# Kernel optimization log

Hardware: AMD Instinct MI355X
Metric: run time of the kernel (lower is better)

## Reference

```python
import jax, jax.numpy as jnp
import numpy as np

N_NODES = 100000   # m for both sparse matmuls (graph adjacency is N x N)
ITERATIONS = 10
ALPHA = 0.1
N_FEATURES = 2000
HIDDEN = 64
N_LABELS = 16
NNZ_FEAT = 5000000
N_EDGES = 3200000


def setup_inputs() -> dict:
    key = jax.random.key(0)
    ks = jax.random.split(key, 10)
    feat_rows = jax.random.randint(ks[0], (NNZ_FEAT,), 0, N_NODES, dtype=jnp.int32)
    feat_cols = jax.random.randint(ks[1], (NNZ_FEAT,), 0, N_FEATURES, dtype=jnp.int32)
    feature_values = jax.random.uniform(ks[2], (NNZ_FEAT,), dtype=jnp.float32)
    edge_rows = jax.random.randint(ks[3], (N_EDGES,), 0, N_NODES, dtype=jnp.int32)
    edge_cols = jax.random.randint(ks[4], (N_EDGES,), 0, N_NODES, dtype=jnp.int32)
    edge_weights = jax.random.uniform(ks[5], (N_EDGES,), dtype=jnp.float32) * (1.0 / 32.0)
    W1 = jax.random.normal(ks[6], (N_FEATURES, HIDDEN), dtype=jnp.float32) * 0.05
    b1 = jax.random.normal(ks[7], (HIDDEN,), dtype=jnp.float32) * 0.05
    W2 = jax.random.normal(ks[8], (HIDDEN, N_LABELS), dtype=jnp.float32) * 0.1
    b2 = jax.random.normal(ks[9], (N_LABELS,), dtype=jnp.float32) * 0.1
    return {"feat_rows": feat_rows, "feat_cols": feat_cols, "feature_values": feature_values,
            "edge_rows": edge_rows, "edge_cols": edge_cols, "edge_weights": edge_weights,
            "W1": W1, "b1": b1, "W2": W2, "b2": b2}


def spmm(rows, cols, vals, matrix, m):
    # sparse [m, k] (COO) @ dense [k, d]: gather rows of dense, scale, scatter-add
    out = matrix[cols] * vals[:, None]          # [nnz, d]
    return jax.ops.segment_sum(out, rows, num_segments=m)


def reference(feat_rows, feat_cols, feature_values, edge_rows, edge_cols,
              edge_weights, W1, b1, W2, b2):
    # layer 1: sparse features [N, F] @ W1 [F, H] + b1  (eval mode: dropout is identity)
    latent1 = spmm(feat_rows, feat_cols, feature_values, W1, N_NODES) + b1  # [N, H]
    latent1 = jax.nn.relu(latent1)
    z = latent1 @ W2 + b2                       # [N, L] local predictions

    def step(p, _):
        new = spmm(edge_rows, edge_cols, edge_weights, p, N_NODES)  # A_hat @ p
        p = (1.0 - ALPHA) * new + ALPHA * z
        return p, None

    preds, _ = jax.lax.scan(step, z, None, length=ITERATIONS)
    return jax.nn.log_softmax(preds, axis=1)
```

## Files before the change

kernel.cpp:

```cpp
#include <hip/hip_runtime.h>

#define N_NODES    100000
#define N_FEATURES 2000
#define HIDDEN     64
#define N_LABELS   16
#define NNZ_FEAT   5000000
#define N_EDGES    3200000
#define ITERS      10
#define ALPHA      0.1f

#define CBSH       9
#define CROWS      (1 << CBSH)
#define NBC        ((N_NODES + CROWS - 1) >> CBSH)
#define TILE       8192
#define NFB        ((NNZ_FEAT + TILE - 1) / TILE)
#define NEB        ((N_EDGES + TILE - 1) / TILE)
#define BCAP       28672

#define EQMUL  1048544.0f
#define EWDEC  (0.028125f / 32767.0f)

__device__ __forceinline__ unsigned short f2bf(float x) {
    unsigned u = __float_as_uint(x);
    u += 0x7FFF + ((u >> 16) & 1);
    return (unsigned short)(u >> 16);
}
__device__ __forceinline__ float bf2f(unsigned short h) {
    return __uint_as_float(((unsigned)h) << 16);
}
__device__ __forceinline__ float bf_lo(unsigned u) { return __uint_as_float(u << 16); }
__device__ __forceinline__ float bf_hi(unsigned u) { return __uint_as_float(u & 0xFFFF0000u); }


__global__ __launch_bounds__(256) void zero_int(int* __restrict__ p, int n) {
    int t = blockIdx.x * 256 + threadIdx.x;
    if (t < n) p[t] = 0;
}

__global__ __launch_bounds__(256) void hist2_k(const int* __restrict__ frows, int nf,
                                               int* __restrict__ cbf,
                                               const int* __restrict__ erows, int ne,
                                               int* __restrict__ cbe) {
    __shared__ int h[NBC];
    for (int i = threadIdx.x; i < NBC; i += 256) h[i] = 0;
    __syncthreads();
    const int* rows; int n; int* dst; int b0, nb;
    if (blockIdx.x < 1280) { rows = frows; n = nf; dst = cbf; b0 = blockIdx.x; nb = 1280; }
    else                   { rows = erows; n = ne; dst = cbe; b0 = blockIdx.x - 1280; nb = 768; }
    int stride = nb * 256;
    for (int i = b0 * 256 + threadIdx.x; i < n; i += stride)
        atomicAdd(&h[rows[i] >> CBSH], 1);
    __syncthreads();
    for (int i = threadIdx.x; i < NBC; i += 256)
        if (h[i]) atomicAdd(&dst[i], h[i]);
}

__global__ __launch_bounds__(256) void scan2_k(const int* __restrict__ cbf,
                                               int* __restrict__ cbasef, int* __restrict__ gbf,
                                               int* __restrict__ frp,
                                               const int* __restrict__ cbe,
                                               int* __restrict__ cbasee, int* __restrict__ gbe,
                                               int* __restrict__ erp) {
    const int* cnt; int* cbase; int* gbcur; int* rp;
    if (blockIdx.x == 0) { cnt = cbf; cbase = cbasef; gbcur = gbf; rp = frp; }
    else                 { cnt = cbe; cbase = cbasee; gbcur = gbe; rp = erp; }
    __shared__ int s[256];
    int t = threadIdx.x;
    int v = (t < NBC) ? cnt[t] : 0;
    s[t] = v;
    __syncthreads();
    for (int off = 1; off < 256; off <<= 1) {
        int a = (t >= off) ? s[t - off] : 0;
        __syncthreads();
        s[t] += a;
        __syncthreads();
    }
    if (t < NBC) { cbase[t] = s[t] - v; gbcur[t] = s[t] - v; }
    if (t == NBC - 1) { cbase[NBC] = s[t]; rp[N_NODES] = s[t]; }
}

__global__ __launch_bounds__(1024) void binA2_k(
    const int* __restrict__ frows, const int* __restrict__ fcols, const float* __restrict__ fvals,
    int* __restrict__ gbf, int* __restrict__ fpk, unsigned short* __restrict__ frl,
    const int* __restrict__ erows, const int* __restrict__ ecols, const float* __restrict__ evals,
    int* __restrict__ gbe, int* __restrict__ epk, unsigned short* __restrict__ erl)
{
    __shared__ int            staged_pk[TILE];
    __shared__ unsigned short staged_rl[TILE];
    __shared__ unsigned char  sbkt[TILE];
    __shared__ int cnt[NBC];
    __shared__ int rstart[NBC];
    __shared__ int gbase[NBC];
    __shared__ int sc[256];

    const int* rows; const int* cols; const float* vals;
    int* gbcur; int* bpk; unsigned short* brl;
    int n, qshift, bfval; float qmul;
    int bid = blockIdx.x;
    if (bid < NFB) {
        rows = frows; cols = fcols; vals = fvals; gbcur = gbf; bpk = fpk; brl = frl;
        n = NNZ_FEAT; qshift = 16; qmul = 0.f; bfval = 1;
    } else {
        bid -= NFB;
        rows = erows; cols = ecols; vals = evals; gbcur = gbe; bpk = epk; brl = erl;
        n = N_EDGES; qshift = 17; qmul = EQMUL; bfval = 0;
    }

    int tid = threadIdx.x;
    int base = bid * TILE;
    int m = n - base; if (m > TILE) m = TILE;

    for (int i = tid; i < NBC; i += 1024) cnt[i] = 0;
    __syncthreads();

    int seq[TILE / 1024];
    int rbuf[TILE / 1024];
    #pragma unroll
    for (int k = 0; k < TILE / 1024; ++k) {
        int j = k * 1024 + tid;
        if (j < m) {
            int r = rows[base + j];
            rbuf[k] = r;
            seq[k] = atomicAdd(&cnt[r >> CBSH], 1);
        }
    }
    __syncthreads();

    if (tid < 256) sc[tid] = (tid < NBC) ? cnt[tid] : 0;
    __syncthreads();
    for (int off = 1; off < 256; off <<= 1) {
        int a = 0;
        if (tid < 256 && tid >= off) a = sc[tid - off];
        __syncthreads();
        if (tid < 256) sc[tid] += a;
        __syncthreads();
    }
    if (tid < NBC) rstart[tid] = sc[tid] - cnt[tid];
    __syncthreads();

    #pragma unroll
    for (int k = 0; k < TILE / 1024; ++k) {
        int j = k * 1024 + tid;
        if (j < m) {
            int r = rbuf[k];
            int b = r >> CBSH;
            float v = vals[base + j];
            int q = bfval ? (int)f2bf(v) : __float2int_rn(v * qmul);
            int slot = rstart[b] + seq[k];
            staged_pk[slot] = (q << qshift) | cols[base + j];
            staged_rl[slot] = (unsigned short)(r & (CROWS - 1));
            sbkt[slot] = (unsigned char)b;
        }
    }
    __syncthreads();

    if (tid < NBC && cnt[tid] > 0) gbase[tid] = atomicAdd(&gbcur[tid], cnt[tid]);
    __syncthreads();

    #pragma unroll
    for (int k = 0; k < TILE / 1024; ++k) {
        int slot = k * 1024 + tid;
        if (slot < m) {
            int b = sbkt[slot];
            int dst = gbase[b] + (slot - rstart[b]);
            bpk[dst] = staged_pk[slot];
            brl[dst] = staged_rl[slot];
        }
    }
}

__global__ __launch_bounds__(1024) void binB3_k(
    const int* __restrict__ fpk, const unsigned short* __restrict__ frl,
    const int* __restrict__ cbasef, int* __restrict__ frp, int* __restrict__ fcw,
    const int* __restrict__ epk, const unsigned short* __restrict__ erl,
    const int* __restrict__ cbasee, int* __restrict__ erp, int* __restrict__ ecw)
{
    const int* bin_pk; const unsigned short* bin_rl; const int* cbase; int* rp; int* cw;
    int b = blockIdx.x;
    if (b < NBC) { bin_pk = fpk; bin_rl = frl; cbase = cbasef; rp = frp; cw = fcw; }
    else { b -= NBC; bin_pk = epk; bin_rl = erl; cbase = cbasee; rp = erp; cw = ecw; }

    int r0 = b << CBSH;
    int nrows = N_NODES - r0; if (nrows > CROWS) nrows = CROWS;
    __shared__ int staged[BCAP];
    __shared__ int hist[CROWS];
    __shared__ int sc[CROWS];
    int t = threadIdx.x;
    if (t < CROWS) hist[t] = 0;
    __syncthreads();
    int s = cbase[b], e = cbase[b + 1];
    int cnt = e - s;
    for (int i = s + t; i < e; i += 1024)
        atomicAdd(&hist[bin_rl[i]], 1);
    __syncthreads();
    if (t < CROWS) sc[t] = hist[t];
    __syncthreads();
    for (int off = 1; off < CROWS; off <<= 1) {
        int a = (t >= off && t < CROWS) ? sc[t - off] : 0;
        __syncthreads();
        if (t < CROWS) sc[t] += a;
        __syncthreads();
    }
    if (t < CROWS) {
        int excl = sc[t] - hist[t];
        if (t < nrows) rp[r0 + t] = excl + s;
        hist[t] = excl;
    }
    __syncthreads();

    if (cnt <= BCAP) {
        for (int i = s + t; i < e; i += 1024) {
            int pos = atomicAdd(&hist[bin_rl[i]], 1);
            staged[pos] = bin_pk[i];
        }
        __syncthreads();
        for (int j = t; j < cnt; j += 1024)
            cw[s + j] = staged[j];
    } else {
        for (int i = s + t; i < e; i += 1024) {
            int pos = atomicAdd(&hist[bin_rl[i]], 1);
            cw[s + pos] = bin_pk[i];
        }
    }
}


__global__ __launch_bounds__(256) void w1_to_bf16(const float* __restrict__ W1,
                                                  unsigned short* __restrict__ W1b) {
    int t = blockIdx.x * 256 + threadIdx.x;
    if (t < N_FEATURES * HIDDEN / 4) {
        float4 v = reinterpret_cast<const float4*>(W1)[t];
        ushort4 o;
        o.x = f2bf(v.x); o.y = f2bf(v.y); o.z = f2bf(v.z); o.w = f2bf(v.w);
        reinterpret_cast<ushort4*>(W1b)[t] = o;
    }
}

__global__ __launch_bounds__(256) void spmm_fused(const int* __restrict__ rp,
                                                  const int* __restrict__ cwp,
                                                  const unsigned short* __restrict__ W1b,
                                                  const float* __restrict__ b1,
                                                  const float* __restrict__ W2,
                                                  const float* __restrict__ b2,
                                                  unsigned short* __restrict__ az,
                                                  unsigned short* __restrict__ pb0) {
    __shared__ float sW2T[N_LABELS * (HIDDEN + 1)];
    __shared__ float sb1[HIDDEN];
    __shared__ float sb2[N_LABELS];
    for (int i = threadIdx.x; i < HIDDEN * N_LABELS; i += 256) {
        int h = i >> 4, l = i & 15;
        sW2T[l * (HIDDEN + 1) + h] = W2[i];
    }
    if (threadIdx.x < HIDDEN) sb1[threadIdx.x] = b1[threadIdx.x];
    if (threadIdx.x < N_LABELS) sb2[threadIdx.x] = b2[threadIdx.x];
    __syncthreads();

    int t = blockIdx.x * 256 + threadIdx.x;
    int row = t >> 3, sl = t & 7;
    if (row >= N_NODES) return;
    int s = rp[row], e = rp[row + 1];
    int hbase = sl * 8;

    float acc[8];
    #pragma unroll
    for (int j = 0; j < 8; ++j) acc[j] = 0.f;

    int i = s;
    for (; i + 3 < e; i += 4) {
        uint4 wv[4]; float vv[4];
        #pragma unroll
        for (int k = 0; k < 4; ++k) {
            int pk = cwp[i + k];
            vv[k] = bf_hi((unsigned)pk);
            wv[k] = *reinterpret_cast<const uint4*>(W1b + (size_t)(pk & 0x7FF) * HIDDEN + hbase);
        }
        #pragma unroll
        for (int k = 0; k < 4; ++k) {
            acc[0] = fmaf(vv[k], bf_lo(wv[k].x), acc[0]);
            acc[1] = fmaf(vv[k], bf_hi(wv[k].x), acc[1]);
            acc[2] = fmaf(vv[k], bf_lo(wv[k].y), acc[2]);
            acc[3] = fmaf(vv[k], bf_hi(wv[k].y), acc[3]);
            acc[4] = fmaf(vv[k], bf_lo(wv[k].z), acc[4]);
            acc[5] = fmaf(vv[k], bf_hi(wv[k].z), acc[5]);
            acc[6] = fmaf(vv[k], bf_lo(wv[k].w), acc[6]);
            acc[7] = fmaf(vv[k], bf_hi(wv[k].w), acc[7]);
        }
    }
    for (; i < e; ++i) {
        int pk = cwp[i];
        float v = bf_hi((unsigned)pk);
        uint4 w = *reinterpret_cast<const uint4*>(W1b + (size_t)(pk & 0x7FF) * HIDDEN + hbase);
        acc[0] = fmaf(v, bf_lo(w.x), acc[0]);
        acc[1] = fmaf(v, bf_hi(w.x), acc[1]);
        acc[2] = fmaf(v, bf_lo(w.y), acc[2]);
        acc[3] = fmaf(v, bf_hi(w.y), acc[3]);
        acc[4] = fmaf(v, bf_lo(w.z), acc[4]);
        acc[5] = fmaf(v, bf_hi(w.z), acc[5]);
        acc[6] = fmaf(v, bf_lo(w.w), acc[6]);
        acc[7] = fmaf(v, bf_hi(w.w), acc[7]);
    }

    float part[16];
    #pragma unroll
    for (int l = 0; l < 16; ++l) part[l] = 0.f;
    #pragma unroll
    for (int j = 0; j < 8; ++j) {
        float a = acc[j] + sb1[hbase + j];
        a = a > 0.f ? a : 0.f;
        #pragma unroll
        for (int l = 0; l < 16; ++l)
            part[l] = fmaf(a, sW2T[l * (HIDDEN + 1) + hbase + j], part[l]);
    }
    #pragma unroll
    for (int l = 0; l < 8; ++l) {
        float lo = __shfl_xor(part[l], 1);
        float hi = __shfl_xor(part[l + 8], 1);
        part[l] = (sl & 1) ? (part[l + 8] + hi) : (part[l] + lo);
    }
    #pragma unroll
    for (int l = 0; l < 4; ++l) {
        float lo = __shfl_xor(part[l], 2);
        float hi = __shfl_xor(part[l + 4], 2);
        part[l] = (sl & 2) ? (part[l + 4] + hi) : (part[l] + lo);
    }
    #pragma unroll
    for (int l = 0; l < 2; ++l) {
        float lo = __shfl_xor(part[l], 4);
        float hi = __shfl_xor(part[l + 2], 4);
        part[l] = (sl & 4) ? (part[l + 2] + hi) : (part[l] + lo);
    }
    int lbase = 8 * (sl & 1) + 4 * ((sl >> 1) & 1) + 2 * ((sl >> 2) & 1);
    float z0 = part[0] + sb2[lbase];
    float z1 = part[1] + sb2[lbase + 1];
    unsigned oz = (unsigned)f2bf(z0) | ((unsigned)f2bf(z1) << 16);
    unsigned oa = (unsigned)f2bf(ALPHA * z0) | ((unsigned)f2bf(ALPHA * z1) << 16);
    *reinterpret_cast<unsigned*>(pb0 + (size_t)row * N_LABELS + lbase) = oz;
    *reinterpret_cast<unsigned*>(az  + (size_t)row * N_LABELS + lbase) = oa;
}

__global__ __launch_bounds__(256) void prop_bf16(const int* __restrict__ rp,
                                                 const int* __restrict__ cwp,
                                                 const unsigned short* __restrict__ az,
                                                 const unsigned short* __restrict__ pin,
                                                 unsigned short* __restrict__ pout) {
    int t = blockIdx.x * 256 + threadIdx.x;
    int row = t >> 2, sub = t & 3;
    if (row >= N_NODES) return;
    int s = rp[row], e = rp[row + 1];
    uint2 azw = *reinterpret_cast<const uint2*>(az + (size_t)row * N_LABELS + sub * 4);
    float a0 = bf_lo(azw.x), a1 = bf_hi(azw.x), a2 = bf_lo(azw.y), a3 = bf_hi(azw.y);
    int i = s;
    if ((i & 1) && i < e) {
        int pk = cwp[i];
        float w = (float)((unsigned)pk >> 17) * EWDEC;
        uint2 q = *reinterpret_cast<const uint2*>(pin + (size_t)(pk & 0x1FFFF) * N_LABELS + sub * 4);
        a0 = fmaf(w, bf_lo(q.x), a0); a1 = fmaf(w, bf_hi(q.x), a1);
        a2 = fmaf(w, bf_lo(q.y), a2); a3 = fmaf(w, bf_hi(q.y), a3);
        ++i;
    }
    for (; i + 7 < e; i += 8) {
        int2 cA = *reinterpret_cast<const int2*>(cwp + i);
        int2 cB = *reinterpret_cast<const int2*>(cwp + i + 2);
        int2 cC = *reinterpret_cast<const int2*>(cwp + i + 4);
        int2 cD = *reinterpret_cast<const int2*>(cwp + i + 6);
        int pks[8] = {cA.x, cA.y, cB.x, cB.y, cC.x, cC.y, cD.x, cD.y};
        uint2 q[8]; float w[8];
        #pragma unroll
        for (int k = 0; k < 8; ++k) {
            int pk = pks[k];
            w[k] = (float)((unsigned)pk >> 17) * EWDEC;
            q[k] = *reinterpret_cast<const uint2*>(pin + (size_t)(pk & 0x1FFFF) * N_LABELS + sub * 4);
        }
        #pragma unroll
        for (int k = 0; k < 8; ++k) {
            a0 = fmaf(w[k], bf_lo(q[k].x), a0); a1 = fmaf(w[k], bf_hi(q[k].x), a1);
            a2 = fmaf(w[k], bf_lo(q[k].y), a2); a3 = fmaf(w[k], bf_hi(q[k].y), a3);
        }
    }
    for (; i < e; ++i) {
        int pk = cwp[i];
        float w = (float)((unsigned)pk >> 17) * EWDEC;
        uint2 q = *reinterpret_cast<const uint2*>(pin + (size_t)(pk & 0x1FFFF) * N_LABELS + sub * 4);
        a0 = fmaf(w, bf_lo(q.x), a0); a1 = fmaf(w, bf_hi(q.x), a1);
        a2 = fmaf(w, bf_lo(q.y), a2); a3 = fmaf(w, bf_hi(q.y), a3);
    }
    uint2 o;
    o.x = (unsigned)f2bf(a0) | ((unsigned)f2bf(a1) << 16);
    o.y = (unsigned)f2bf(a2) | ((unsigned)f2bf(a3) << 16);
    *reinterpret_cast<uint2*>(pout + (size_t)row * N_LABELS + sub * 4) = o;
}

__global__ __launch_bounds__(256) void prop_final(const int* __restrict__ rp,
                                                  const int* __restrict__ cwp,
                                                  const unsigned short* __restrict__ az,
                                                  const unsigned short* __restrict__ pin,
                                                  float* __restrict__ out) {
    int t = blockIdx.x * 256 + threadIdx.x;
    int row = t >> 2, sub = t & 3;
    if (row >= N_NODES) return;
    int s = rp[row], e = rp[row + 1];
    uint2 azw = *reinterpret_cast<const uint2*>(az + (size_t)row * N_LABELS + sub * 4);
    float a0 = bf_lo(azw.x), a1 = bf_hi(azw.x), a2 = bf_lo(azw.y), a3 = bf_hi(azw.y);
    int i = s;
    if ((i & 1) && i < e) {
        int pk = cwp[i];
        float w = (float)((unsigned)pk >> 17) * EWDEC;
        uint2 q = *reinterpret_cast<const uint2*>(pin + (size_t)(pk & 0x1FFFF) * N_LABELS + sub * 4);
        a0 = fmaf(w, bf_lo(q.x), a0); a1 = fmaf(w, bf_hi(q.x), a1);
        a2 = fmaf(w, bf_lo(q.y), a2); a3 = fmaf(w, bf_hi(q.y), a3);
        ++i;
    }
    for (; i + 7 < e; i += 8) {
        int2 cA = *reinterpret_cast<const int2*>(cwp + i);
        int2 cB = *reinterpret_cast<const int2*>(cwp + i + 2);
        int2 cC = *reinterpret_cast<const int2*>(cwp + i + 4);
        int2 cD = *reinterpret_cast<const int2*>(cwp + i + 6);
        int pks[8] = {cA.x, cA.y, cB.x, cB.y, cC.x, cC.y, cD.x, cD.y};
        uint2 q[8]; float w[8];
        #pragma unroll
        for (int k = 0; k < 8; ++k) {
            int pk = pks[k];
            w[k] = (float)((unsigned)pk >> 17) * EWDEC;
            q[k] = *reinterpret_cast<const uint2*>(pin + (size_t)(pk & 0x1FFFF) * N_LABELS + sub * 4);
        }
        #pragma unroll
        for (int k = 0; k < 8; ++k) {
            a0 = fmaf(w[k], bf_lo(q[k].x), a0); a1 = fmaf(w[k], bf_hi(q[k].x), a1);
            a2 = fmaf(w[k], bf_lo(q[k].y), a2); a3 = fmaf(w[k], bf_hi(q[k].y), a3);
        }
    }
    for (; i < e; ++i) {
        int pk = cwp[i];
        float w = (float)((unsigned)pk >> 17) * EWDEC;
        uint2 q = *reinterpret_cast<const uint2*>(pin + (size_t)(pk & 0x1FFFF) * N_LABELS + sub * 4);
        a0 = fmaf(w, bf_lo(q.x), a0); a1 = fmaf(w, bf_hi(q.x), a1);
        a2 = fmaf(w, bf_lo(q.y), a2); a3 = fmaf(w, bf_hi(q.y), a3);
    }
    float m = fmaxf(fmaxf(a0, a1), fmaxf(a2, a3));
    m = fmaxf(m, __shfl_xor(m, 1));
    m = fmaxf(m, __shfl_xor(m, 2));
    float ssum = __expf(a0 - m) + __expf(a1 - m) + __expf(a2 - m) + __expf(a3 - m);
    ssum += __shfl_xor(ssum, 1);
    ssum += __shfl_xor(ssum, 2);
    float lse = m + __logf(ssum);
    float4 o = make_float4(a0 - lse, a1 - lse, a2 - lse, a3 - lse);
    *reinterpret_cast<float4*>(out + (size_t)row * N_LABELS + sub * 4) = o;
}


__global__ __launch_bounds__(256) void zero_f4(float4* __restrict__ p, int n4) {
    int t = blockIdx.x * 256 + threadIdx.x;
    if (t < n4) p[t] = make_float4(0.f, 0.f, 0.f, 0.f);
}

__global__ __launch_bounds__(256) void spmm_feat_atomic(
    const int* __restrict__ rows, const int* __restrict__ cols,
    const float* __restrict__ vals, const float* __restrict__ W1,
    float* __restrict__ latent)
{
    long long t = (long long)blockIdx.x * 256 + threadIdx.x;
    if (t >= (long long)NNZ_FEAT * 16) return;
    int e  = (int)(t >> 4);
    int dg = (int)(t & 15);
    int r = rows[e]; int c = cols[e]; float v = vals[e];
    float4 w = *reinterpret_cast<const float4*>(W1 + (size_t)c * HIDDEN + dg * 4);
    float* dst = latent + (size_t)r * HIDDEN + dg * 4;
    atomicAdd(dst + 0, v * w.x); atomicAdd(dst + 1, v * w.y);
    atomicAdd(dst + 2, v * w.z); atomicAdd(dst + 3, v * w.w);
}

__global__ __launch_bounds__(256) void compute_z(const float* __restrict__ latent,
                                                 const float* __restrict__ b1,
                                                 const float* __restrict__ W2,
                                                 const float* __restrict__ b2,
                                                 float* __restrict__ z) {
    __shared__ float sW2[HIDDEN * N_LABELS];
    __shared__ float sb1[HIDDEN];
    for (int i = threadIdx.x; i < HIDDEN * N_LABELS; i += 256) sW2[i] = W2[i];
    if (threadIdx.x < HIDDEN) sb1[threadIdx.x] = b1[threadIdx.x];
    __syncthreads();
    int t = blockIdx.x * 256 + threadIdx.x;
    int node = t >> 4;
    int l = t & 15;
    if (node >= N_NODES) return;
    float acc = b2[l];
    const float* lat = latent + (size_t)node * HIDDEN;
    #pragma unroll 8
    for (int h = 0; h < HIDDEN; ++h) {
        float a = lat[h] + sb1[h];
        a = a > 0.f ? a : 0.f;
        acc = fmaf(a, sW2[h * N_LABELS + l], acc);
    }
    z[(size_t)node * N_LABELS + l] = acc;
}

__global__ __launch_bounds__(256) void init_acc(const float* __restrict__ z,
                                                float* __restrict__ acc) {
    int t = blockIdx.x * 256 + threadIdx.x;
    if (t < N_NODES * N_LABELS / 4) {
        float4 zv = reinterpret_cast<const float4*>(z)[t];
        reinterpret_cast<float4*>(acc)[t] =
            make_float4(ALPHA * zv.x, ALPHA * zv.y, ALPHA * zv.z, ALPHA * zv.w);
    }
}

__global__ __launch_bounds__(256) void edge_scatter(
    const int* __restrict__ rows, const int* __restrict__ cols,
    const float* __restrict__ w, const float* __restrict__ p,
    float* __restrict__ acc)
{
    long long t = (long long)blockIdx.x * 256 + threadIdx.x;
    if (t >= (long long)N_EDGES * 4) return;
    int e = (int)(t >> 2);
    int part = (int)(t & 3);
    int r = rows[e]; int c = cols[e];
    float wt = w[e] * (1.0f - ALPHA);
    float4 pv = *reinterpret_cast<const float4*>(p + (size_t)c * N_LABELS + part * 4);
    float* dst = acc + (size_t)r * N_LABELS + part * 4;
    atomicAdd(dst + 0, wt * pv.x); atomicAdd(dst + 1, wt * pv.y);
    atomicAdd(dst + 2, wt * pv.z); atomicAdd(dst + 3, wt * pv.w);
}

__global__ __launch_bounds__(256) void logsoftmax_k(const float* __restrict__ p,
                                                    float* __restrict__ out) {
    int node = blockIdx.x * 256 + threadIdx.x;
    if (node >= N_NODES) return;
    const float4* src = reinterpret_cast<const float4*>(p + (size_t)node * N_LABELS);
    float4 a = src[0], b = src[1], c = src[2], d = src[3];
    float x[16] = {a.x,a.y,a.z,a.w, b.x,b.y,b.z,b.w, c.x,c.y,c.z,c.w, d.x,d.y,d.z,d.w};
    float m = x[0];
    #pragma unroll
    for (int i = 1; i < 16; ++i) m = fmaxf(m, x[i]);
    float s = 0.f;
    #pragma unroll
    for (int i = 0; i < 16; ++i) s += expf(x[i] - m);
    float lse = m + logf(s);
    float4* o = reinterpret_cast<float4*>(out + (size_t)node * N_LABELS);
    o[0] = make_float4(x[0]-lse,  x[1]-lse,  x[2]-lse,  x[3]-lse);
    o[1] = make_float4(x[4]-lse,  x[5]-lse,  x[6]-lse,  x[7]-lse);
    o[2] = make_float4(x[8]-lse,  x[9]-lse,  x[10]-lse, x[11]-lse);
    o[3] = make_float4(x[12]-lse, x[13]-lse, x[14]-lse, x[15]-lse);
}


extern "C" void kernel_launch(void* const* d_in, const int* in_sizes, int n_in,
                              void* d_out, int out_size, void* d_ws, size_t ws_size,
                              hipStream_t stream)
{
    const int*   feat_rows = (const int*)d_in[0];
    const int*   feat_cols = (const int*)d_in[1];
    const float* feat_vals = (const float*)d_in[2];
    const int*   edge_rows = (const int*)d_in[3];
    const int*   edge_cols = (const int*)d_in[4];
    const float* edge_w    = (const float*)d_in[5];
    const float* W1 = (const float*)d_in[6];
    const float* b1 = (const float*)d_in[7];
    const float* W2 = (const float*)d_in[8];
    const float* b2 = (const float*)d_in[9];
    float* out = (float*)d_out;

    size_t need = 0;
    size_t o_feat_cw = need; need += (size_t)NNZ_FEAT;
    size_t o_edge_cw = need; need += (size_t)N_EDGES;
    size_t o_latent  = need; need += (size_t)N_NODES * HIDDEN;
    size_t o_z       = need; need += (size_t)N_NODES * N_LABELS;
    size_t o_p0      = need; need += (size_t)N_NODES * N_LABELS;
    size_t o_p1      = need; need += (size_t)N_NODES * N_LABELS;
    size_t o_frp     = need; need += N_NODES + 1;
    size_t o_erp     = need; need += N_NODES + 1;
    size_t o_w1b     = need; need += (size_t)N_FEATURES * HIDDEN / 2;
    size_t o_ebin_pk = need; need += (size_t)N_EDGES;
    size_t o_ebin_rl = need; need += (size_t)N_EDGES / 2;
    size_t o_cbf     = need; need += NBC;
    size_t o_cbe     = need; need += NBC;
    size_t o_cbasef  = need; need += NBC + 1;
    size_t o_cbasee  = need; need += NBC + 1;
    size_t o_gbf     = need; need += NBC;
    size_t o_gbe     = need; need += NBC;
    size_t need_bytes = need * 4 + 64;

    float* base = (float*)d_ws;
    float* latent = base + o_latent;
    float* z  = base + o_z;
    float* p0 = base + o_p0;
    float* p1 = base + o_p1;

    if (ws_size >= need_bytes) {
        int* feat_cw = (int*)(base + o_feat_cw);
        int* edge_cw = (int*)(base + o_edge_cw);
        int* feat_rp = (int*)(base + o_frp);
        int* edge_rp = (int*)(base + o_erp);
        unsigned short* W1b = (unsigned short*)(base + o_w1b);
        int* cbf    = (int*)(base + o_cbf);
        int* cbe    = (int*)(base + o_cbe);
        int* cbasef = (int*)(base + o_cbasef);
        int* cbasee = (int*)(base + o_cbasee);
        int* gbf    = (int*)(base + o_gbf);
        int* gbe    = (int*)(base + o_gbe);
        int*            fbin_pk = (int*)(base + o_latent);
        unsigned short* fbin_rl = (unsigned short*)(base + o_z);
        int*            ebin_pk = (int*)(base + o_ebin_pk);
        unsigned short* ebin_rl = (unsigned short*)(base + o_ebin_rl);
        unsigned short* az  = (unsigned short*)z;
        unsigned short* pb0 = (unsigned short*)p0;
        unsigned short* pb1 = (unsigned short*)p1;

        w1_to_bf16<<<(N_FEATURES * HIDDEN / 4 + 255) / 256, 256, 0, stream>>>(W1, W1b);
        zero_int<<<2, 256, 0, stream>>>(cbf, 2 * NBC);
        hist2_k<<<2048, 256, 0, stream>>>(feat_rows, NNZ_FEAT, cbf, edge_rows, N_EDGES, cbe);
        scan2_k<<<2, 256, 0, stream>>>(cbf, cbasef, gbf, feat_rp, cbe, cbasee, gbe, edge_rp);
        binA2_k<<<NFB + NEB, 1024, 0, stream>>>(
            feat_rows, feat_cols, feat_vals, gbf, fbin_pk, fbin_rl,
            edge_rows, edge_cols, edge_w, gbe, ebin_pk, ebin_rl);
        binB3_k<<<2 * NBC, 1024, 0, stream>>>(
            fbin_pk, fbin_rl, cbasef, feat_rp, feat_cw,
            ebin_pk, ebin_rl, cbasee, edge_rp, edge_cw);

        spmm_fused<<<(N_NODES * 8 + 255) / 256, 256, 0, stream>>>(
            feat_rp, feat_cw, W1b, b1, W2, b2, az, pb0);

        const unsigned short* pin = pb0;
        int pgrid = (N_NODES * 4 + 255) / 256;
        for (int it = 0; it < ITERS - 1; ++it) {
            unsigned short* pout = (it & 1) ? pb0 : pb1;
            prop_bf16<<<pgrid, 256, 0, stream>>>(edge_rp, edge_cw, az, pin, pout);
            pin = pout;
        }
        prop_final<<<pgrid, 256, 0, stream>>>(edge_rp, edge_cw, az, pin, out);
    } else {
        int n4 = N_NODES * HIDDEN / 4;
        zero_f4<<<(n4 + 255) / 256, 256, 0, stream>>>((float4*)latent, n4);
        long long total = (long long)NNZ_FEAT * 16;
        spmm_feat_atomic<<<(int)((total + 255) / 256), 256, 0, stream>>>(
            feat_rows, feat_cols, feat_vals, W1, latent);
        compute_z<<<N_NODES * 16 / 256, 256, 0, stream>>>(latent, b1, W2, b2, z);
        const float* pin = z;
        float* bufs[2] = {p0, p1};
        for (int it = 0; it < ITERS; ++it) {
            float* pout = bufs[it & 1];
            init_acc<<<(N_NODES * N_LABELS / 4 + 255) / 256, 256, 0, stream>>>(z, pout);
            long long tot = (long long)N_EDGES * 4;
            edge_scatter<<<(int)((tot + 255) / 256), 256, 0, stream>>>(
                edge_rows, edge_cols, edge_w, pin, pout);
            pin = pout;
        }
        logsoftmax_k<<<(N_NODES + 255) / 256, 256, 0, stream>>>(pin, out);
    }
}
```

Measured before the change: 489.0 us.

## Sort rows by degree for load balance and quantize W1 to fp8

Adds a counting-sort pass (length histogram, scan, scatter) that builds permutations grouping rows of similar nnz count. The feature SpMM and all propagation kernels then process rows in that order, so lanes in a wavefront get balanced work. W1 is also stored as a scaled custom fp8 (e4m3-style with a 16x prescale), halving gather bytes per nonzero. This adds three small kernels and lowers precision of W1, and the permuted order scatters output writes.

```diff
diff --git a/kernel.cpp b/kernel.cpp
--- a/kernel.cpp
+++ b/kernel.cpp
@@ -16,6 +16,7 @@
 #define NFB        ((NNZ_FEAT + TILE - 1) / TILE)
 #define NEB        ((N_EDGES + TILE - 1) / TILE)
 #define BCAP       28672
+#define LMAX       256
 
 #define EQMUL  1048544.0f
 #define EWDEC  (0.028125f / 32767.0f)
@@ -25,11 +26,26 @@
     u += 0x7FFF + ((u >> 16) & 1);
     return (unsigned short)(u >> 16);
 }
-__device__ __forceinline__ float bf2f(unsigned short h) {
-    return __uint_as_float(((unsigned)h) << 16);
-}
 __device__ __forceinline__ float bf_lo(unsigned u) { return __uint_as_float(u << 16); }
 __device__ __forceinline__ float bf_hi(unsigned u) { return __uint_as_float(u & 0xFFFF0000u); }
+
+__device__ __forceinline__ unsigned char f2fp8(float x) {
+    float a = fabsf(x) * 16.0f;
+    a = fminf(fmaxf(a, 0.015625f), 448.0f);
+    unsigned u = __float_as_uint(a) + 0x80000;
+    int v11 = (int)((u >> 20) & 0x7FF) - 960;
+    v11 = v11 < 8 ? 8 : (v11 > 126 ? 126 : v11);
+    return (unsigned char)(v11 | ((__float_as_uint(x) >> 24) & 0x80));
+}
+#if __has_builtin(__builtin_amdgcn_cvt_f32_fp8)
+#define FP8DEC(w, s) __builtin_amdgcn_cvt_f32_fp8((w), (s))
+#else
+__device__ __forceinline__ float fp8dec_sw(unsigned w, int s) {
+    unsigned u = (w >> (8 * s)) & 0xFF;
+    return __uint_as_float((((u & 0x7F) + 960) << 20) | ((u & 0x80) << 24));
+}
+#define FP8DEC(w, s) fp8dec_sw((w), (s))
+#endif
 
 
 __global__ __launch_bounds__(256) void zero_int(int* __restrict__ p, int n) {
@@ -224,21 +240,79 @@
     }
 }
 
-
-__global__ __launch_bounds__(256) void w1_to_bf16(const float* __restrict__ W1,
-                                                  unsigned short* __restrict__ W1b) {
+__global__ __launch_bounds__(256) void lenhist2_k(const int* __restrict__ frp,
+                                                  const int* __restrict__ erp,
+                                                  int* __restrict__ fl, int* __restrict__ el) {
+    __shared__ int h[LMAX];
+    for (int i = threadIdx.x; i < LMAX; i += 256) h[i] = 0;
+    __syncthreads();
+    int nb2 = gridDim.x >> 1;
+    bool isF = blockIdx.x < nb2;
+    const int* rp = isF ? frp : erp;
+    int* dst = isF ? fl : el;
+    int b0 = isF ? blockIdx.x : blockIdx.x - nb2;
+    for (int i = b0 * 256 + threadIdx.x; i < N_NODES; i += nb2 * 256) {
+        int len = rp[i + 1] - rp[i]; if (len >= LMAX) len = LMAX - 1;
+        atomicAdd(&h[len], 1);
+    }
+    __syncthreads();
+    for (int i = threadIdx.x; i < LMAX; i += 256)
+        if (h[i]) atomicAdd(&dst[i], h[i]);
+}
+
+__global__ __launch_bounds__(LMAX) void lenscan2_k(const int* __restrict__ fl,
+                                                   int* __restrict__ fcur,
+                                                   const int* __restrict__ el,
+                                                   int* __restrict__ ecur) {
+    const int* cnt = (blockIdx.x == 0) ? fl : el;
+    int* cur = (blockIdx.x == 0) ? fcur : ecur;
+    __shared__ int s[LMAX];
+    int t = threadIdx.x;
+    int v = cnt[t];
+    s[t] = v;
+    __syncthreads();
+    for (int off = 1; off < LMAX; off <<= 1) {
+        int a = (t >= off) ? s[t - off] : 0;
+        __syncthreads();
+        s[t] += a;
+        __syncthreads();
+    }
+    cur[t] = s[t] - v;
+}
+
+__global__ __launch_bounds__(256) void permscatter2_k(const int* __restrict__ frp,
+                                                      int* __restrict__ fcur, int* __restrict__ fperm,
+                                                      const int* __restrict__ erp,
+                                                      int* __restrict__ ecur, int* __restrict__ eperm) {
+    int nb2 = gridDim.x >> 1;
+    bool isF = blockIdx.x < nb2;
+    const int* rp = isF ? frp : erp;
+    int* cur = isF ? fcur : ecur;
+    int* pm = isF ? fperm : eperm;
+    int b0 = isF ? blockIdx.x : blockIdx.x - nb2;
+    for (int i = b0 * 256 + threadIdx.x; i < N_NODES; i += nb2 * 256) {
+        int len = rp[i + 1] - rp[i]; if (len >= LMAX) len = LMAX - 1;
+        int pos = atomicAdd(&cur[len], 1);
+        pm[pos] = i;
+    }
+}
+
+
+__global__ __launch_bounds__(256) void w1_to_fp8(const float* __restrict__ W1,
+                                                 unsigned char* __restrict__ W1q) {
     int t = blockIdx.x * 256 + threadIdx.x;
     if (t < N_FEATURES * HIDDEN / 4) {
         float4 v = reinterpret_cast<const float4*>(W1)[t];
-        ushort4 o;
-        o.x = f2bf(v.x); o.y = f2bf(v.y); o.z = f2bf(v.z); o.w = f2bf(v.w);
-        reinterpret_cast<ushort4*>(W1b)[t] = o;
+        uchar4 o;
+        o.x = f2fp8(v.x); o.y = f2fp8(v.y); o.z = f2fp8(v.z); o.w = f2fp8(v.w);
+        reinterpret_cast<uchar4*>(W1q)[t] = o;
     }
 }
 
 __global__ __launch_bounds__(256) void spmm_fused(const int* __restrict__ rp,
                                                   const int* __restrict__ cwp,
-                                                  const unsigned short* __restrict__ W1b,
+                                                  const unsigned char* __restrict__ W1q,
+                                                  const int* __restrict__ fperm,
                                                   const float* __restrict__ b1,
                                                   const float* __restrict__ W2,
                                                   const float* __restrict__ b2,
@@ -256,8 +330,9 @@
     __syncthreads();
 
     int t = blockIdx.x * 256 + threadIdx.x;
-    int row = t >> 3, sl = t & 7;
-    if (row >= N_NODES) return;
+    int ridx = t >> 3, sl = t & 7;
+    if (ridx >= N_NODES) return;
+    int row = fperm[ridx];
     int s = rp[row], e = rp[row + 1];
     int hbase = sl * 8;
 
@@ -267,37 +342,37 @@
 
     int i = s;
     for (; i + 3 < e; i += 4) {
-        uint4 wv[4]; float vv[4];
+        uint2 wv[4]; float vv[4];
         #pragma unroll
         for (int k = 0; k < 4; ++k) {
             int pk = cwp[i + k];
             vv[k] = bf_hi((unsigned)pk);
-            wv[k] = *reinterpret_cast<const uint4*>(W1b + (size_t)(pk & 0x7FF) * HIDDEN + hbase);
+            wv[k] = *reinterpret_cast<const uint2*>(W1q + (size_t)(pk & 0x7FF) * HIDDEN + hbase);
         }
         #pragma unroll
         for (int k = 0; k < 4; ++k) {
-            acc[0] = fmaf(vv[k], bf_lo(wv[k].x), acc[0]);
-            acc[1] = fmaf(vv[k], bf_hi(wv[k].x), acc[1]);
-            acc[2] = fmaf(vv[k], bf_lo(wv[k].y), acc[2]);
-            acc[3] = fmaf(vv[k], bf_hi(wv[k].y), acc[3]);
-            acc[4] = fmaf(vv[k], bf_lo(wv[k].z), acc[4]);
-            acc[5] = fmaf(vv[k], bf_hi(wv[k].z), acc[5]);
-            acc[6] = fmaf(vv[k], bf_lo(wv[k].w), acc[6]);
-            acc[7] = fmaf(vv[k], bf_hi(wv[k].w), acc[7]);
+            acc[0] = fmaf(vv[k], FP8DEC(wv[k].x, 0), acc[0]);
+            acc[1] = fmaf(vv[k], FP8DEC(wv[k].x, 1), acc[1]);
+            acc[2] = fmaf(vv[k], FP8DEC(wv[k].x, 2), acc[2]);
+            acc[3] = fmaf(vv[k], FP8DEC(wv[k].x, 3), acc[3]);
+            acc[4] = fmaf(vv[k], FP8DEC(wv[k].y, 0), acc[4]);
+            acc[5] = fmaf(vv[k], FP8DEC(wv[k].y, 1), acc[5]);
+            acc[6] = fmaf(vv[k], FP8DEC(wv[k].y, 2), acc[6]);
+            acc[7] = fmaf(vv[k], FP8DEC(wv[k].y, 3), acc[7]);
         }
     }
     for (; i < e; ++i) {
         int pk = cwp[i];
         float v = bf_hi((unsigned)pk);
-        uint4 w = *reinterpret_cast<const uint4*>(W1b + (size_t)(pk & 0x7FF) * HIDDEN + hbase);
-        acc[0] = fmaf(v, bf_lo(w.x), acc[0]);
-        acc[1] = fmaf(v, bf_hi(w.x), acc[1]);
-        acc[2] = fmaf(v, bf_lo(w.y), acc[2]);
-        acc[3] = fmaf(v, bf_hi(w.y), acc[3]);
-        acc[4] = fmaf(v, bf_lo(w.z), acc[4]);
-        acc[5] = fmaf(v, bf_hi(w.z), acc[5]);
-        acc[6] = fmaf(v, bf_lo(w.w), acc[6]);
-        acc[7] = fmaf(v, bf_hi(w.w), acc[7]);
+        uint2 w = *reinterpret_cast<const uint2*>(W1q + (size_t)(pk & 0x7FF) * HIDDEN + hbase);
+        acc[0] = fmaf(v, FP8DEC(w.x, 0), acc[0]);
+        acc[1] = fmaf(v, FP8DEC(w.x, 1), acc[1]);
+        acc[2] = fmaf(v, FP8DEC(w.x, 2), acc[2]);
+        acc[3] = fmaf(v, FP8DEC(w.x, 3), acc[3]);
+        acc[4] = fmaf(v, FP8DEC(w.y, 0), acc[4]);
+        acc[5] = fmaf(v, FP8DEC(w.y, 1), acc[5]);
+        acc[6] = fmaf(v, FP8DEC(w.y, 2), acc[6]);
+        acc[7] = fmaf(v, FP8DEC(w.y, 3), acc[7]);
     }
 
     float part[16];
@@ -305,7 +380,7 @@
     for (int l = 0; l < 16; ++l) part[l] = 0.f;
     #pragma unroll
     for (int j = 0; j < 8; ++j) {
-        float a = acc[j] + sb1[hbase + j];
+        float a = fmaf(acc[j], 0.0625f, sb1[hbase + j]);
         a = a > 0.f ? a : 0.f;
         #pragma unroll
         for (int l = 0; l < 16; ++l)
@@ -340,12 +415,14 @@
 
 __global__ __launch_bounds__(256) void prop_bf16(const int* __restrict__ rp,
                                                  const int* __restrict__ cwp,
+                                                 const int* __restrict__ eperm,
                                                  const unsigned short* __restrict__ az,
                                                  const unsigned short* __restrict__ pin,
                                                  unsigned short* __restrict__ pout) {
     int t = blockIdx.x * 256 + threadIdx.x;
-    int row = t >> 2, sub = t & 3;
-    if (row >= N_NODES) return;
+    int ridx = t >> 2, sub = t & 3;
+    if (ridx >= N_NODES) return;
+    int row = eperm[ridx];
     int s = rp[row], e = rp[row + 1];
     uint2 azw = *reinterpret_cast<const uint2*>(az + (size_t)row * N_LABELS + sub * 4);
     float a0 = bf_lo(azw.x), a1 = bf_hi(azw.x), a2 = bf_lo(azw.y), a3 = bf_hi(azw.y);
@@ -392,12 +469,14 @@
 
 __global__ __launch_bounds__(256) void prop_final(const int* __restrict__ rp,
                                                   const int* __restrict__ cwp,
+                                                  const int* __restrict__ eperm,
                                                   const unsigned short* __restrict__ az,
                                                   const unsigned short* __restrict__ pin,
                                                   float* __restrict__ out) {
     int t = blockIdx.x * 256 + threadIdx.x;
-    int row = t >> 2, sub = t & 3;
-    if (row >= N_NODES) return;
+    int ridx = t >> 2, sub = t & 3;
+    if (ridx >= N_NODES) return;
+    int row = eperm[ridx];
     int s = rp[row], e = rp[row + 1];
     uint2 azw = *reinterpret_cast<const uint2*>(az + (size_t)row * N_LABELS + sub * 4);
     float a0 = bf_lo(azw.x), a1 = bf_hi(azw.x), a2 = bf_lo(azw.y), a3 = bf_hi(azw.y);
@@ -568,9 +647,15 @@
     size_t o_p1      = need; need += (size_t)N_NODES * N_LABELS;
     size_t o_frp     = need; need += N_NODES + 1;
     size_t o_erp     = need; need += N_NODES + 1;
-    size_t o_w1b     = need; need += (size_t)N_FEATURES * HIDDEN / 2;
+    size_t o_w1q     = need; need += (size_t)N_FEATURES * HIDDEN / 4;
     size_t o_ebin_pk = need; need += (size_t)N_EDGES;
     size_t o_ebin_rl = need; need += (size_t)N_EDGES / 2;
+    size_t o_fperm   = need; need += N_NODES;
+    size_t o_eperm   = need; need += N_NODES;
+    size_t o_fl      = need; need += LMAX;
+    size_t o_el      = need; need += LMAX;
+    size_t o_fcur    = need; need += LMAX;
+    size_t o_ecur    = need; need += LMAX;
     size_t o_cbf     = need; need += NBC;
     size_t o_cbe     = need; need += NBC;
     size_t o_cbasef  = need; need += NBC + 1;
@@ -590,7 +675,13 @@
         int* edge_cw = (int*)(base + o_edge_cw);
         int* feat_rp = (int*)(base + o_frp);
         int* edge_rp = (int*)(base + o_erp);
-        unsigned short* W1b = (unsigned short*)(base + o_w1b);
+        unsigned char* W1q = (unsigned char*)(base + o_w1q);
+        int* fperm  = (int*)(base + o_fperm);
+        int* eperm  = (int*)(base + o_eperm);
+        int* fl     = (int*)(base + o_fl);
+        int* el     = (int*)(base + o_el);
+        int* fcur   = (int*)(base + o_fcur);
+        int* ecur   = (int*)(base + o_ecur);
         int* cbf    = (int*)(base + o_cbf);
         int* cbe    = (int*)(base + o_cbe);
         int* cbasef = (int*)(base + o_cbasef);
@@ -605,8 +696,9 @@
         unsigned short* pb0 = (unsigned short*)p0;
         unsigned short* pb1 = (unsigned short*)p1;
 
-        w1_to_bf16<<<(N_FEATURES * HIDDEN / 4 + 255) / 256, 256, 0, stream>>>(W1, W1b);
+        w1_to_fp8<<<(N_FEATURES * HIDDEN / 4 + 255) / 256, 256, 0, stream>>>(W1, W1q);
         zero_int<<<2, 256, 0, stream>>>(cbf, 2 * NBC);
+        zero_int<<<2, 256, 0, stream>>>(fl, 2 * LMAX);
         hist2_k<<<2048, 256, 0, stream>>>(feat_rows, NNZ_FEAT, cbf, edge_rows, N_EDGES, cbe);
         scan2_k<<<2, 256, 0, stream>>>(cbf, cbasef, gbf, feat_rp, cbe, cbasee, gbe, edge_rp);
         binA2_k<<<NFB + NEB, 1024, 0, stream>>>(
@@ -616,17 +708,21 @@
             fbin_pk, fbin_rl, cbasef, feat_rp, feat_cw,
             ebin_pk, ebin_rl, cbasee, edge_rp, edge_cw);
 
+        lenhist2_k<<<782, 256, 0, stream>>>(feat_rp, edge_rp, fl, el);
+        lenscan2_k<<<2, LMAX, 0, stream>>>(fl, fcur, el, ecur);
+        permscatter2_k<<<782, 256, 0, stream>>>(feat_rp, fcur, fperm, edge_rp, ecur, eperm);
+
         spmm_fused<<<(N_NODES * 8 + 255) / 256, 256, 0, stream>>>(
-            feat_rp, feat_cw, W1b, b1, W2, b2, az, pb0);
+            feat_rp, feat_cw, W1q, fperm, b1, W2, b2, az, pb0);
 
         const unsigned short* pin = pb0;
         int pgrid = (N_NODES * 4 + 255) / 256;
         for (int it = 0; it < ITERS - 1; ++it) {
             unsigned short* pout = (it & 1) ? pb0 : pb1;
-            prop_bf16<<<pgrid, 256, 0, stream>>>(edge_rp, edge_cw, az, pin, pout);
+            prop_bf16<<<pgrid, 256, 0, stream>>>(edge_rp, edge_cw, eperm, az, pin, pout);
             pin = pout;
         }
-        prop_final<<<pgrid, 256, 0, stream>>>(edge_rp, edge_cw, az, pin, out);
+        prop_final<<<pgrid, 256, 0, stream>>>(edge_rp, edge_cw, eperm, az, pin, out);
     } else {
         int n4 = N_NODES * HIDDEN / 4;
         zero_f4<<<(n4 + 255) / 256, 256, 0, stream>>>((float4*)latent, n4);
```

Result: slower. 840.9 us (+72.0%).
